# Optimization experiments

Measured on AMD Instinct MI355X. Metric: run time of the kernel, lower is better.

Reference implementation:

```python
import jax, jax.numpy as jnp
import numpy as np

B, S, HID = 2, 2048, 2048
NH, NKV = 16, 4
HD = HID // NH            # 128
N_REP = NH // NKV          # 4
THETA = 10000.0
NEG = -1e9


def _rope_tables(position_ids):
    # inv_freq: [HD/2]
    inv_freq = 1.0 / (THETA ** (jnp.arange(0, HD, 2, dtype=jnp.float32) / HD))
    freqs = position_ids.astype(jnp.float32)[..., None] * inv_freq  # [B,S,HD/2]
    emb = jnp.concatenate([freqs, freqs], axis=-1)                  # [B,S,HD]
    return jnp.cos(emb), jnp.sin(emb)


def _rotate_half(x):
    return jnp.concatenate([-x[..., HD // 2:], x[..., :HD // 2]], axis=-1)


def setup_inputs() -> dict:
    key = jax.random.key(0)
    k1, k2, k3 = jax.random.split(key, 3)
    hidden_states = jax.random.normal(k1, (B, S, HID), dtype=jnp.float32)
    w_qkv = jax.random.normal(k2, (HID + 2 * NKV * HD, HID), dtype=jnp.float32) * 0.02
    w_out = jax.random.normal(k3, (HID, HID), dtype=jnp.float32) * 0.02
    causal = jnp.tril(jnp.ones((S, S), dtype=bool))
    attention_mask = jnp.where(causal, 0.0, NEG).astype(jnp.float32)
    attention_mask = jnp.broadcast_to(attention_mask[None, None], (B, 1, S, S))
    position_ids = jnp.broadcast_to(jnp.arange(S, dtype=jnp.int64), (B, S))
    return {"hidden_states": hidden_states, "w_qkv": w_qkv, "w_out": w_out,
            "attention_mask": attention_mask, "position_ids": position_ids}


def reference(hidden_states, w_qkv, w_out, attention_mask, position_ids):
    bsz, q_len, _ = hidden_states.shape
    qkv = hidden_states @ w_qkv.T                                   # [B,S,HID+2*NKV*HD]
    q, k, v = jnp.split(qkv, [HID, HID + NKV * HD], axis=-1)
    q = q.reshape(bsz, q_len, NH, HD).transpose(0, 2, 1, 3)         # [B,NH,S,HD]
    k = k.reshape(bsz, q_len, NKV, HD).transpose(0, 2, 1, 3)        # [B,NKV,S,HD]
    v = v.reshape(bsz, q_len, NKV, HD).transpose(0, 2, 1, 3)

    cos, sin = _rope_tables(position_ids)                           # [B,S,HD]
    cos, sin = cos[:, None], sin[:, None]                           # unsqueeze head dim
    q = q * cos + _rotate_half(q) * sin
    k = k * cos + _rotate_half(k) * sin

    # GQA: repeat KV heads to match query heads (repeat_kv)
    k = jnp.repeat(k, N_REP, axis=1)                                # [B,NH,S,HD]
    v = jnp.repeat(v, N_REP, axis=1)

    scale = 1.0 / jnp.sqrt(jnp.float32(HD))
    scores = jnp.einsum('bhqd,bhkd->bhqk', q, k) * scale
    scores = scores + attention_mask                                # [B,NH,S,S]
    attn = jax.nn.softmax(scores.astype(jnp.float32), axis=-1).astype(q.dtype)
    out = jnp.einsum('bhqk,bhkd->bhqd', attn, v)                    # [B,NH,S,HD]
    out = out.transpose(0, 2, 1, 3).reshape(bsz, q_len, HID)
    return out @ w_out.T
```

## Files before the change

kernel.cpp:

```cpp
#include <hip/hip_runtime.h>
#include <hip/hip_bf16.h>
#include <math.h>

#define S_LEN   2048
#define HIDDEN  2048
#define NHEADS  16
#define NKVH    4
#define HDIM    128

typedef short  short8  __attribute__((ext_vector_type(8)));
typedef float  floatx4 __attribute__((ext_vector_type(4)));
typedef __hip_bfloat16 bf16;

__device__ inline void async_copy16(const void* g, void* l) {
  __builtin_amdgcn_global_load_lds((__attribute__((address_space(1))) void*)(g),
                                   (__attribute__((address_space(3))) void*)(l),
                                   16, 0, 0);
}

__device__ inline unsigned short cvt1(float x) {
  bf16 t = __float2bfloat16(x);
  return *reinterpret_cast<unsigned short*>(&t);
}
__device__ inline float us2f(unsigned short u) {
  unsigned int v = ((unsigned int)u) << 16;
  return *reinterpret_cast<float*>(&v);
}

#define N8_H  1048576
#define N8_WQ  786432
#define N8_WO  524288
__global__ __launch_bounds__(256) void cvt_all(const float* __restrict__ h,
                                               const float* __restrict__ wq,
                                               const float* __restrict__ wo,
                                               unsigned short* __restrict__ dst) {
  const int i = blockIdx.x * 256 + threadIdx.x;
  if (i >= N8_H + N8_WQ + N8_WO) return;
  const float* src; int j;
  if (i < N8_H)              { src = h;  j = i; }
  else if (i < N8_H + N8_WQ) { src = wq; j = i - N8_H; }
  else                       { src = wo; j = i - N8_H - N8_WQ; }
  const float4 a = reinterpret_cast<const float4*>(src)[j * 2];
  const float4 b = reinterpret_cast<const float4*>(src)[j * 2 + 1];
  unsigned short o[8] = {cvt1(a.x), cvt1(a.y), cvt1(a.z), cvt1(a.w),
                         cvt1(b.x), cvt1(b.y), cvt1(b.z), cvt1(b.w)};
  *reinterpret_cast<short8*>(dst + (size_t)i * 8) = *reinterpret_cast<short8*>(o);
}

__global__ __launch_bounds__(256) void cvt_wo(const float* __restrict__ wo,
                                              unsigned short* __restrict__ dst) {
  const int i = blockIdx.x * 256 + threadIdx.x;
  if (i >= N8_WO) return;
  const float4 a = reinterpret_cast<const float4*>(wo)[i * 2];
  const float4 b = reinterpret_cast<const float4*>(wo)[i * 2 + 1];
  unsigned short o[8] = {cvt1(a.x), cvt1(a.y), cvt1(a.z), cvt1(a.w),
                         cvt1(b.x), cvt1(b.y), cvt1(b.z), cvt1(b.w)};
  *reinterpret_cast<short8*>(dst + (size_t)i * 8) = *reinterpret_cast<short8*>(o);
}

template<int MODE>
__global__ __launch_bounds__(512, 2) void gemm8(const bf16* __restrict__ A,
                                                const bf16* __restrict__ B,
                                                bf16* __restrict__ qbuf,
                                                bf16* __restrict__ kbuf,
                                                bf16* __restrict__ vtbuf,
                                                float* __restrict__ Cout)
{
  constexpr int K      = 2048;
  constexpr int BM     = (MODE == 0) ? 256 : 128;
  constexpr int BN     = 256;
  constexpr int MF     = BM / 32;
  constexpr int AI     = BM / 128;
  constexpr int ABYTES = BM * 64;
  constexpr int SLOT   = (BM + BN) * 64;
  constexpr int NSTEP  = K / 32;

  __shared__ __align__(16) unsigned short smem[SLOT * 4 / 2];
  char* smb = (char*)smem;

  const int bn = blockIdx.x, bm = blockIdx.y;
  const int t = threadIdx.x, w = t >> 6, lane = t & 63;
  const int m16 = lane & 15, quad = lane >> 4;
  const int wmr = (w >> 2) * (BM / 2);
  const int wn  = w & 3;

  int bcol[4];
#pragma unroll
  for (int ni = 0; ni < 4; ++ni)
    bcol[ni] = (MODE == 0)
             ? ((wn >> 1) * 128 + (wn & 1) * 32 + (ni & 1) * 16 + (ni >> 1) * 64)
             : (wn * 64 + ni * 16);

  int afo[MF], bfo[4];
#pragma unroll
  for (int mf = 0; mf < MF; ++mf) {
    const int r = wmr + mf * 16 + m16;
    afo[mf] = r * 64 + ((quad ^ ((r >> 1) & 3)) << 4);
  }
#pragma unroll
  for (int ni = 0; ni < 4; ++ni) {
    const int r = bcol[ni] + m16;
    bfo[ni] = ABYTES + r * 64 + ((quad ^ ((r >> 1) & 3)) << 4);
  }

  const bf16* srcA[AI]; int dstA[AI];
#pragma unroll
  for (int j = 0; j < AI; ++j) {
    const int ci  = w * AI + j;
    const int row = ci * 16 + (lane >> 2);
    const int sl  = (lane & 3) ^ ((row >> 1) & 3);
    srcA[j] = A + (size_t)(bm * BM + row) * K + sl * 8;
    dstA[j] = ci * 1024;
  }
  const bf16* srcB[2]; int dstB[2];
#pragma unroll
  for (int j = 0; j < 2; ++j) {
    const int ci  = w * 2 + j;
    const int row = ci * 16 + (lane >> 2);
    const int sl  = (lane & 3) ^ ((row >> 1) & 3);
    srcB[j] = B + (size_t)(bn * BN + row) * K + sl * 8;
    dstB[j] = ABYTES + ci * 1024;
  }

  auto stage = [&](int step, int slotbyte) {
#pragma unroll
    for (int j = 0; j < AI; ++j)
      async_copy16(srcA[j] + step * 32, smb + slotbyte + dstA[j]);
#pragma unroll
    for (int j = 0; j < 2; ++j)
      async_copy16(srcB[j] + step * 32, smb + slotbyte + dstB[j]);
  };

  const floatx4 zf = {0.f, 0.f, 0.f, 0.f};
  floatx4 acc[MF][4];
#pragma unroll
  for (int mf = 0; mf < MF; ++mf)
#pragma unroll
    for (int ni = 0; ni < 4; ++ni) acc[mf][ni] = zf;

  stage(0, 0); stage(1, SLOT); stage(2, 2 * SLOT);

#pragma unroll 4
  for (int s = 0; s < NSTEP; ++s) {
    __builtin_amdgcn_sched_barrier(0);
    if constexpr (MODE == 0) asm volatile("s_waitcnt vmcnt(8)" ::: "memory");
    else                     asm volatile("s_waitcnt vmcnt(6)" ::: "memory");
    __builtin_amdgcn_s_barrier();
    __builtin_amdgcn_sched_barrier(0);
    const int sb = (s & 3) * SLOT;
    short8 af[MF], bfr[4];
#pragma unroll
    for (int mf = 0; mf < MF; ++mf)
      af[mf] = *reinterpret_cast<const short8*>(smb + sb + afo[mf]);
#pragma unroll
    for (int ni = 0; ni < 4; ++ni)
      bfr[ni] = *reinterpret_cast<const short8*>(smb + sb + bfo[ni]);
    stage((s + 3) & (NSTEP - 1), ((s + 3) & 3) * SLOT);
    __builtin_amdgcn_s_setprio(1);
#pragma unroll
    for (int mf = 0; mf < MF; ++mf)
#pragma unroll
      for (int ni = 0; ni < 4; ++ni)
        acc[mf][ni] = __builtin_amdgcn_mfma_f32_16x16x32_bf16(af[mf], bfr[ni], acc[mf][ni], 0, 0, 0);
    __builtin_amdgcn_s_setprio(0);
  }
  __builtin_amdgcn_s_waitcnt(0);

  if constexpr (MODE == 1) {
#pragma unroll
    for (int mf = 0; mf < MF; ++mf)
#pragma unroll
      for (int ni = 0; ni < 4; ++ni) {
        const int row0 = bm * BM + wmr + mf * 16 + quad * 4;
        const int col  = bn * BN + bcol[ni] + m16;
#pragma unroll
        for (int r = 0; r < 4; ++r)
          Cout[(size_t)(row0 + r) * HIDDEN + col] = acc[mf][ni][r];
      }
  } else {
    const int colbase = bn * BN;
    if (colbase < HIDDEN + NKVH * HDIM) {
      const bool isQ = (colbase < HIDDEN);
      const float post = isQ ? 0.08838834764831845f : 1.0f;
      float invf[2];
#pragma unroll
      for (int p = 0; p < 2; ++p)
        invf[p] = exp2f((float)((wn & 1) * 32 + p * 16 + m16) * -0.2076205059f);
#pragma unroll
      for (int mf = 0; mf < MF; ++mf) {
        const int row0 = bm * BM + wmr + mf * 16 + quad * 4;
#pragma unroll
        for (int r = 0; r < 4; ++r) {
          const int m = row0 + r;
          const int b = m >> 11, s = m & 2047;
          float sn[2], cs[2];
          __sincosf((float)s * invf[0], &sn[0], &cs[0]);
          __sincosf((float)s * invf[1], &sn[1], &cs[1]);
#pragma unroll
          for (int ni = 0; ni < 4; ++ni) {
            const int p = ni & 1;
            const float v  = acc[mf][ni][r];
            const float v2 = acc[mf][ni ^ 2][r];
            const float rot = ((ni < 2) ? (v * cs[p] - v2 * sn[p])
                                        : (v * cs[p] + v2 * sn[p])) * post;
            const int col = colbase + bcol[ni] + m16;
            if (isQ) {
              const int hh = col >> 7, d = col & 127;
              qbuf[(((size_t)(b * NHEADS + hh)) * S_LEN + s) * HDIM + d] = __float2bfloat16(rot);
            } else {
              const int nn = col - HIDDEN; const int hh = nn >> 7, d = nn & 127;
              kbuf[(((size_t)(b * NKVH + hh)) * S_LEN + s) * HDIM + d] = __float2bfloat16(rot);
            }
          }
        }
      }
    } else {
#pragma unroll
      for (int mf = 0; mf < MF; ++mf)
#pragma unroll
        for (int ni = 0; ni < 4; ++ni) {
          const int col = colbase + bcol[ni] + m16;
          const int nn = col - HIDDEN - NKVH * HDIM;
          const int hh = nn >> 7, d = nn & 127;
          const int row0 = bm * BM + wmr + mf * 16 + quad * 4;
#pragma unroll
          for (int r = 0; r < 4; ++r) {
            const int m = row0 + r;
            const int b = m >> 11, s = m & 2047;
            vtbuf[(((size_t)(b * NKVH + hh)) * HDIM + d) * S_LEN + s] =
                __float2bfloat16(acc[mf][ni][r]);
          }
        }
    }
  }
}

__global__ __launch_bounds__(256) void attn_partial(const bf16* __restrict__ qbuf,
                                                    const bf16* __restrict__ kbuf,
                                                    const bf16* __restrict__ vtbuf,
                                                    unsigned short* __restrict__ pnum,
                                                    float* __restrict__ plsum,
                                                    bf16* __restrict__ abuf)
{
  __shared__ unsigned short Ks[2][4096];
  __shared__ unsigned short Vs[2][4096];
  __shared__ unsigned short Ps[4][1280];
  const int sidx = 159 - blockIdx.x;
  int i2, c, nch;
  if (sidx < 16)      { i2 = sidx;                       c = 0;           nch = 1; }
  else if (sidx < 48) { const int q = sidx - 16; i2 = 16 + (q >> 1); c = q & 1; nch = 2; }
  else if (sidx < 96) { const int q = sidx - 48; i2 = 32 + q / 3;    c = q % 3; nch = 3; }
  else                { const int q = sidx - 96; i2 = 48 + (q >> 2); c = q & 3; nch = 4; }
  const int len = i2 + 1;
  const int k0 = (c * len) / nch, k1 = ((c + 1) * len) / nch;
  const int kvh = blockIdx.y, b = blockIdx.z;
  const int t = threadIdx.x, w = t >> 6, lane = t & 63;
  const int m16 = lane & 15, quad = lane >> 4;
  const int h = kvh * 4 + w;

  const bf16* Qp = qbuf + (((size_t)(b * NHEADS + h)) * S_LEN + i2 * 32 + m16) * HDIM;
  short8 qf[2][4];
#pragma unroll
  for (int T = 0; T < 2; ++T)
#pragma unroll
    for (int cc = 0; cc < 4; ++cc)
      qf[T][cc] = *reinterpret_cast<const short8*>(Qp + (size_t)T * 16 * HDIM + cc * 32 + quad * 8);

  const bf16* Kp  = kbuf  + ((size_t)(b * NKVH + kvh)) * S_LEN * HDIM;
  const bf16* Vtp = vtbuf + ((size_t)(b * NKVH + kvh)) * HDIM * S_LEN;

  const int kk = lane >> 4, cK = lane & 15;
  const int rKa = w * 8 + kk, rKb = rKa + 4;
  const int offKa = rKa * 128 + ((cK ^ (rKa & 7)) * 8);
  const int offKb = rKb * 128 + ((cK ^ (rKb & 7)) * 8);
  const int dd = lane >> 2, cV = lane & 3;
  const int dVa = w * 32 + dd, dVb = dVa + 16;
  const int offVa = dVa * 2048 + ((cV ^ ((dVa >> 1) & 3)) * 8);
  const int offVb = dVb * 2048 + ((cV ^ ((dVb >> 1) & 3)) * 8);

  const floatx4 zf = {0.f, 0.f, 0.f, 0.f};
  floatx4 oacc[2][8];
#pragma unroll
  for (int T = 0; T < 2; ++T)
#pragma unroll
    for (int d = 0; d < 8; ++d) oacc[T][d] = zf;
  floatx4 lacc[2] = {zf, zf};
  unsigned short ones_s[8] = {0x3F80,0x3F80,0x3F80,0x3F80,0x3F80,0x3F80,0x3F80,0x3F80};
  const short8 ones = *reinterpret_cast<short8*>(ones_s);

  unsigned short* Pw = &Ps[w][0];

  {
    const int ks = k0 * 32;
    async_copy16(Kp + (size_t)ks * 128 + offKa, &Ks[0][w * 1024]);
    async_copy16(Kp + (size_t)ks * 128 + offKb, &Ks[0][w * 1024 + 512]);
    async_copy16(Vtp + ks + offVa, &Vs[0][w * 1024]);
    async_copy16(Vtp + ks + offVb, &Vs[0][w * 1024 + 512]);
  }
  __syncthreads();

  for (int ki = k0; ki < k1; ++ki) {
    const int buf = (ki - k0) & 1;
    if (ki + 1 < k1) {
      const int ks = (ki + 1) * 32;
      async_copy16(Kp + (size_t)ks * 128 + offKa, &Ks[buf ^ 1][w * 1024]);
      async_copy16(Kp + (size_t)ks * 128 + offKb, &Ks[buf ^ 1][w * 1024 + 512]);
      async_copy16(Vtp + ks + offVa, &Vs[buf ^ 1][w * 1024]);
      async_copy16(Vtp + ks + offVb, &Vs[buf ^ 1][w * 1024 + 512]);
    }
    const int ks = ki * 32;
    floatx4 s00 = zf, s01 = zf, s10 = zf, s11 = zf;
#pragma unroll
    for (int cc = 0; cc < 4; ++cc) {
      const int sw = ((cc * 4 + quad) ^ (m16 & 7)) * 8;
      short8 kf0 = *reinterpret_cast<const short8*>(&Ks[buf][m16 * 128 + sw]);
      short8 kf1 = *reinterpret_cast<const short8*>(&Ks[buf][(16 + m16) * 128 + sw]);
      s00 = __builtin_amdgcn_mfma_f32_16x16x32_bf16(qf[0][cc], kf0, s00, 0, 0, 0);
      s01 = __builtin_amdgcn_mfma_f32_16x16x32_bf16(qf[0][cc], kf1, s01, 0, 0, 0);
      s10 = __builtin_amdgcn_mfma_f32_16x16x32_bf16(qf[1][cc], kf0, s10, 0, 0, 0);
      s11 = __builtin_amdgcn_mfma_f32_16x16x32_bf16(qf[1][cc], kf1, s11, 0, 0, 0);
    }
#pragma unroll
    for (int T = 0; T < 2; ++T) {
      const floatx4& sa = T ? s10 : s00;
      const floatx4& sb = T ? s11 : s01;
#pragma unroll
      for (int r = 0; r < 4; ++r) {
        const int row = i2 * 32 + T * 16 + quad * 4 + r;
        const float p0 = (ks + m16      > row) ? 0.f : __expf(sa[r]);
        const float p1 = (ks + 16 + m16 > row) ? 0.f : __expf(sb[r]);
        Pw[(T * 16 + quad * 4 + r) * 40 + m16]      = cvt1(p0);
        Pw[(T * 16 + quad * 4 + r) * 40 + 16 + m16] = cvt1(p1);
      }
    }
    const short8 pa0 = *reinterpret_cast<const short8*>(&Pw[m16 * 40 + quad * 8]);
    const short8 pa1 = *reinterpret_cast<const short8*>(&Pw[(16 + m16) * 40 + quad * 8]);
    lacc[0] = __builtin_amdgcn_mfma_f32_16x16x32_bf16(pa0, ones, lacc[0], 0, 0, 0);
    lacc[1] = __builtin_amdgcn_mfma_f32_16x16x32_bf16(pa1, ones, lacc[1], 0, 0, 0);
#pragma unroll
    for (int dt = 0; dt < 8; ++dt) {
      short8 vfr = *reinterpret_cast<const short8*>(
          &Vs[buf][(dt * 16 + m16) * 32 + ((quad ^ ((m16 >> 1) & 3)) * 8)]);
      oacc[0][dt] = __builtin_amdgcn_mfma_f32_16x16x32_bf16(pa0, vfr, oacc[0][dt], 0, 0, 0);
      oacc[1][dt] = __builtin_amdgcn_mfma_f32_16x16x32_bf16(pa1, vfr, oacc[1][dt], 0, 0, 0);
    }
    __syncthreads();
  }

  if (nch == 1) {
#pragma unroll
    for (int T = 0; T < 2; ++T) {
      float invl[4];
#pragma unroll
      for (int r = 0; r < 4; ++r) invl[r] = 1.0f / lacc[T][r];
      bf16* op = abuf + (((size_t)b * S_LEN + i2 * 32 + T * 16 + quad * 4) * NHEADS + h) * HDIM + m16;
#pragma unroll
      for (int dt = 0; dt < 8; ++dt)
#pragma unroll
        for (int r = 0; r < 4; ++r)
          op[(size_t)r * NHEADS * HDIM + dt * 16] = __float2bfloat16(oacc[T][dt][r] * invl[r]);
    }
  } else {
    const int base = (i2 < 32) ? (i2 - 16) * 2
                   : (i2 < 48) ? 32 + (i2 - 32) * 3
                               : 80 + (i2 - 48) * 4;
    const int slot = (b * NHEADS + h) * 144 + base + c;
    unsigned short* np = pnum + (size_t)slot * 4096;
#pragma unroll
    for (int T = 0; T < 2; ++T)
#pragma unroll
      for (int dt = 0; dt < 8; ++dt)
#pragma unroll
        for (int r = 0; r < 4; ++r)
          np[(T * 16 + quad * 4 + r) * 128 + dt * 16 + m16] = cvt1(oacc[T][dt][r]);
    if (m16 == 0) {
#pragma unroll
      for (int T = 0; T < 2; ++T)
#pragma unroll
        for (int r = 0; r < 4; ++r)
          plsum[slot * 32 + T * 16 + quad * 4 + r] = lacc[T][r];
    }
  }
}

__global__ __launch_bounds__(256) void attn_combine(const unsigned short* __restrict__ pnum,
                                                    const float* __restrict__ plsum,
                                                    bf16* __restrict__ abuf)
{
  const int i2 = 16 + blockIdx.x;
  const int h = blockIdx.y, b = blockIdx.z;
  const int nch  = (i2 >= 48) ? 4 : (i2 >= 32) ? 3 : 2;
  const int base = (i2 < 32) ? (i2 - 16) * 2
                 : (i2 < 48) ? 32 + (i2 - 32) * 3
                             : 80 + (i2 - 48) * 4;
  const int hb = (b * NHEADS + h) * 144 + base;
  const int t = threadIdx.x, row16 = t >> 4, c0 = (t & 15) * 8;
#pragma unroll
  for (int T = 0; T < 2; ++T) {
    const int lr = T * 16 + row16;
    float acc[8] = {0.f,0.f,0.f,0.f,0.f,0.f,0.f,0.f};
    float lsum = 0.f;
    for (int c = 0; c < nch; ++c) {
      const unsigned short* np = pnum + (size_t)(hb + c) * 4096 + lr * 128 + c0;
      const short8 v = *reinterpret_cast<const short8*>(np);
#pragma unroll
      for (int j = 0; j < 8; ++j) acc[j] += us2f(((unsigned short*)&v)[j]);
      lsum += plsum[(hb + c) * 32 + lr];
    }
    const float invl = 1.0f / lsum;
    unsigned short o[8];
#pragma unroll
    for (int j = 0; j < 8; ++j) o[j] = cvt1(acc[j] * invl);
    *reinterpret_cast<short8*>(abuf + (((size_t)b * S_LEN + i2 * 32 + lr) * NHEADS + h) * HDIM + c0)
        = *reinterpret_cast<short8*>(o);
  }
}

extern "C" void kernel_launch(void* const* d_in, const int* in_sizes, int n_in,
                              void* d_out, int out_size, void* d_ws, size_t ws_size,
                              hipStream_t stream) {
  const float* hidden_f = (const float*)d_in[0];
  const float* wqkv_f   = (const float*)d_in[1];
  const float* wout_f   = (const float*)d_in[2];
  float* out = (float*)d_out;

  char* ws = (char*)d_ws;
  bf16* hbf    = (bf16*)(ws);
  bf16* wqkvbf = (bf16*)(ws + 16777216);
  bf16* woutbf = (bf16*)(ws + 29360128);
  bf16* qbuf   = (bf16*)(ws + 37748736);
  bf16* kbuf   = (bf16*)(ws + 54525952);
  bf16* vtbuf  = (bf16*)(ws + 58720256);
  bf16* abuf   = (bf16*)(ws + 62914560);
  unsigned short* pnum = (unsigned short*)(ws);
  float* plsum = (float*)(ws + 79691776);

  cvt_all<<<9216, 256, 0, stream>>>(hidden_f, wqkv_f, wout_f, (unsigned short*)ws);

  gemm8<0><<<dim3(12, 16), 512, 0, stream>>>(hbf, wqkvbf, 4096 ? qbuf : qbuf, kbuf, vtbuf, nullptr);
  attn_partial<<<dim3(160, 4, 2), 256, 0, stream>>>(qbuf, kbuf, vtbuf, pnum, plsum, abuf);
  attn_combine<<<dim3(48, 16, 2), 256, 0, stream>>>(pnum, plsum, abuf);
  cvt_wo<<<2048, 256, 0, stream>>>(wout_f, (unsigned short*)(ws + 29360128));
  gemm8<1><<<dim3(8, 32), 512, 0, stream>>>(abuf, woutbf, nullptr, nullptr, nullptr, out);
}
```

Baseline: 308.5 us.

## Widen attention blocks to 64 query rows with 8 waves sharing K/V tiles

The attention partial kernel now processes 64 query rows per block using 512 threads (8 waves: 4 heads × 2 row halves), so each K/V tile loaded into LDS serves twice as many query rows. The work split, partial-sum slot layout and combine kernel are remapped to the new 64-row granularity. This halves K/V global traffic per query row but also halves the block count, which may reduce occupancy and load balance on a large GPU.

```diff
diff --git a/kernel.cpp b/kernel.cpp
--- a/kernel.cpp
+++ b/kernel.cpp
@@ -235,7 +235,7 @@
   }
 }
 
-__global__ __launch_bounds__(256) void attn_partial(const bf16* __restrict__ qbuf,
+__global__ __launch_bounds__(512) void attn_partial(const bf16* __restrict__ qbuf,
                                                     const bf16* __restrict__ kbuf,
                                                     const bf16* __restrict__ vtbuf,
                                                     unsigned short* __restrict__ pnum,
@@ -244,21 +244,23 @@
 {
   __shared__ unsigned short Ks[2][4096];
   __shared__ unsigned short Vs[2][4096];
-  __shared__ unsigned short Ps[4][1280];
-  const int sidx = 159 - blockIdx.x;
-  int i2, c, nch;
-  if (sidx < 16)      { i2 = sidx;                       c = 0;           nch = 1; }
-  else if (sidx < 48) { const int q = sidx - 16; i2 = 16 + (q >> 1); c = q & 1; nch = 2; }
-  else if (sidx < 96) { const int q = sidx - 48; i2 = 32 + q / 3;    c = q % 3; nch = 3; }
-  else                { const int q = sidx - 96; i2 = 48 + (q >> 2); c = q & 3; nch = 4; }
-  const int len = i2 + 1;
+  __shared__ unsigned short Ps[8][1280];
+  const int sidx = 79 - blockIdx.x;
+  int i4, c, nch;
+  if (sidx < 8)       { i4 = sidx;                    c = 0;         nch = 1; }
+  else if (sidx < 24) { const int q = sidx - 8;  i4 = 8  + (q >> 1); c = q & 1; nch = 2; }
+  else if (sidx < 48) { const int q = sidx - 24; i4 = 16 + q / 3;    c = q % 3; nch = 3; }
+  else                { const int q = sidx - 48; i4 = 24 + (q >> 2); c = q & 3; nch = 4; }
+  const int len = 2 * (i4 + 1);
   const int k0 = (c * len) / nch, k1 = ((c + 1) * len) / nch;
   const int kvh = blockIdx.y, b = blockIdx.z;
   const int t = threadIdx.x, w = t >> 6, lane = t & 63;
   const int m16 = lane & 15, quad = lane >> 4;
-  const int h = kvh * 4 + w;
-
-  const bf16* Qp = qbuf + (((size_t)(b * NHEADS + h)) * S_LEN + i2 * 32 + m16) * HDIM;
+  const int half = w >> 2;
+  const int h = kvh * 4 + (w & 3);
+  const int qrow0 = i4 * 64 + half * 32;
+
+  const bf16* Qp = qbuf + (((size_t)(b * NHEADS + h)) * S_LEN + qrow0 + m16) * HDIM;
   short8 qf[2][4];
 #pragma unroll
   for (int T = 0; T < 2; ++T)
@@ -269,14 +271,12 @@
   const bf16* Kp  = kbuf  + ((size_t)(b * NKVH + kvh)) * S_LEN * HDIM;
   const bf16* Vtp = vtbuf + ((size_t)(b * NKVH + kvh)) * HDIM * S_LEN;
 
-  const int kk = lane >> 4, cK = lane & 15;
-  const int rKa = w * 8 + kk, rKb = rKa + 4;
-  const int offKa = rKa * 128 + ((cK ^ (rKa & 7)) * 8);
-  const int offKb = rKb * 128 + ((cK ^ (rKb & 7)) * 8);
-  const int dd = lane >> 2, cV = lane & 3;
-  const int dVa = w * 32 + dd, dVb = dVa + 16;
-  const int offVa = dVa * 2048 + ((cV ^ ((dVa >> 1) & 3)) * 8);
-  const int offVb = dVb * 2048 + ((cV ^ ((dVb >> 1) & 3)) * 8);
+  const int rK = w * 4 + (lane >> 4);
+  const int cK = lane & 15;
+  const int offK = rK * 128 + ((cK ^ (rK & 7)) * 8);
+  const int dV = w * 16 + (lane >> 2);
+  const int cV = lane & 3;
+  const int offV = dV * 2048 + ((cV ^ ((dV >> 1) & 3)) * 8);
 
   const floatx4 zf = {0.f, 0.f, 0.f, 0.f};
   floatx4 oacc[2][8];
@@ -292,10 +292,8 @@
 
   {
     const int ks = k0 * 32;
-    async_copy16(Kp + (size_t)ks * 128 + offKa, &Ks[0][w * 1024]);
-    async_copy16(Kp + (size_t)ks * 128 + offKb, &Ks[0][w * 1024 + 512]);
-    async_copy16(Vtp + ks + offVa, &Vs[0][w * 1024]);
-    async_copy16(Vtp + ks + offVb, &Vs[0][w * 1024 + 512]);
+    async_copy16(Kp + (size_t)ks * 128 + offK, &Ks[0][w * 512]);
+    async_copy16(Vtp + ks + offV, &Vs[0][w * 512]);
   }
   __syncthreads();
 
@@ -303,10 +301,8 @@
     const int buf = (ki - k0) & 1;
     if (ki + 1 < k1) {
       const int ks = (ki + 1) * 32;
-      async_copy16(Kp + (size_t)ks * 128 + offKa, &Ks[buf ^ 1][w * 1024]);
-      async_copy16(Kp + (size_t)ks * 128 + offKb, &Ks[buf ^ 1][w * 1024 + 512]);
-      async_copy16(Vtp + ks + offVa, &Vs[buf ^ 1][w * 1024]);
-      async_copy16(Vtp + ks + offVb, &Vs[buf ^ 1][w * 1024 + 512]);
+      async_copy16(Kp + (size_t)ks * 128 + offK, &Ks[buf ^ 1][w * 512]);
+      async_copy16(Vtp + ks + offV, &Vs[buf ^ 1][w * 512]);
     }
     const int ks = ki * 32;
     floatx4 s00 = zf, s01 = zf, s10 = zf, s11 = zf;
@@ -326,7 +322,7 @@
       const floatx4& sb = T ? s11 : s01;
 #pragma unroll
       for (int r = 0; r < 4; ++r) {
-        const int row = i2 * 32 + T * 16 + quad * 4 + r;
+        const int row = qrow0 + T * 16 + quad * 4 + r;
         const float p0 = (ks + m16      > row) ? 0.f : __expf(sa[r]);
         const float p1 = (ks + 16 + m16 > row) ? 0.f : __expf(sb[r]);
         Pw[(T * 16 + quad * 4 + r) * 40 + m16]      = cvt1(p0);
@@ -353,7 +349,7 @@
       float invl[4];
 #pragma unroll
       for (int r = 0; r < 4; ++r) invl[r] = 1.0f / lacc[T][r];
-      bf16* op = abuf + (((size_t)b * S_LEN + i2 * 32 + T * 16 + quad * 4) * NHEADS + h) * HDIM + m16;
+      bf16* op = abuf + (((size_t)b * S_LEN + qrow0 + T * 16 + quad * 4) * NHEADS + h) * HDIM + m16;
 #pragma unroll
       for (int dt = 0; dt < 8; ++dt)
 #pragma unroll
@@ -361,24 +357,24 @@
           op[(size_t)r * NHEADS * HDIM + dt * 16] = __float2bfloat16(oacc[T][dt][r] * invl[r]);
     }
   } else {
-    const int base = (i2 < 32) ? (i2 - 16) * 2
-                   : (i2 < 48) ? 32 + (i2 - 32) * 3
-                               : 80 + (i2 - 48) * 4;
-    const int slot = (b * NHEADS + h) * 144 + base + c;
-    unsigned short* np = pnum + (size_t)slot * 4096;
+    const int base = (i4 < 16) ? (i4 - 8) * 2
+                   : (i4 < 24) ? 16 + (i4 - 16) * 3
+                               : 40 + (i4 - 24) * 4;
+    const int slot = (b * NHEADS + h) * 72 + base + c;
+    unsigned short* np = pnum + (size_t)slot * 8192;
 #pragma unroll
     for (int T = 0; T < 2; ++T)
 #pragma unroll
       for (int dt = 0; dt < 8; ++dt)
 #pragma unroll
         for (int r = 0; r < 4; ++r)
-          np[(T * 16 + quad * 4 + r) * 128 + dt * 16 + m16] = cvt1(oacc[T][dt][r]);
+          np[(half * 32 + T * 16 + quad * 4 + r) * 128 + dt * 16 + m16] = cvt1(oacc[T][dt][r]);
     if (m16 == 0) {
 #pragma unroll
       for (int T = 0; T < 2; ++T)
 #pragma unroll
         for (int r = 0; r < 4; ++r)
-          plsum[slot * 32 + T * 16 + quad * 4 + r] = lacc[T][r];
+          plsum[(size_t)slot * 64 + half * 32 + T * 16 + quad * 4 + r] = lacc[T][r];
     }
   }
 }
@@ -387,31 +383,31 @@
                                                     const float* __restrict__ plsum,
                                                     bf16* __restrict__ abuf)
 {
-  const int i2 = 16 + blockIdx.x;
+  const int i4 = 8 + blockIdx.x;
   const int h = blockIdx.y, b = blockIdx.z;
-  const int nch  = (i2 >= 48) ? 4 : (i2 >= 32) ? 3 : 2;
-  const int base = (i2 < 32) ? (i2 - 16) * 2
-                 : (i2 < 48) ? 32 + (i2 - 32) * 3
-                             : 80 + (i2 - 48) * 4;
-  const int hb = (b * NHEADS + h) * 144 + base;
+  const int nch  = (i4 < 16) ? 2 : (i4 < 24) ? 3 : 4;
+  const int base = (i4 < 16) ? (i4 - 8) * 2
+                 : (i4 < 24) ? 16 + (i4 - 16) * 3
+                             : 40 + (i4 - 24) * 4;
+  const int hb = (b * NHEADS + h) * 72 + base;
   const int t = threadIdx.x, row16 = t >> 4, c0 = (t & 15) * 8;
 #pragma unroll
-  for (int T = 0; T < 2; ++T) {
+  for (int T = 0; T < 4; ++T) {
     const int lr = T * 16 + row16;
     float acc[8] = {0.f,0.f,0.f,0.f,0.f,0.f,0.f,0.f};
     float lsum = 0.f;
     for (int c = 0; c < nch; ++c) {
-      const unsigned short* np = pnum + (size_t)(hb + c) * 4096 + lr * 128 + c0;
+      const unsigned short* np = pnum + (size_t)(hb + c) * 8192 + lr * 128 + c0;
       const short8 v = *reinterpret_cast<const short8*>(np);
 #pragma unroll
       for (int j = 0; j < 8; ++j) acc[j] += us2f(((unsigned short*)&v)[j]);
-      lsum += plsum[(hb + c) * 32 + lr];
+      lsum += plsum[(size_t)(hb + c) * 64 + lr];
     }
     const float invl = 1.0f / lsum;
     unsigned short o[8];
 #pragma unroll
     for (int j = 0; j < 8; ++j) o[j] = cvt1(acc[j] * invl);
-    *reinterpret_cast<short8*>(abuf + (((size_t)b * S_LEN + i2 * 32 + lr) * NHEADS + h) * HDIM + c0)
+    *reinterpret_cast<short8*>(abuf + (((size_t)b * S_LEN + i4 * 64 + lr) * NHEADS + h) * HDIM + c0)
         = *reinterpret_cast<short8*>(o);
   }
 }
@@ -437,9 +433,9 @@
 
   cvt_all<<<9216, 256, 0, stream>>>(hidden_f, wqkv_f, wout_f, (unsigned short*)ws);
 
-  gemm8<0><<<dim3(12, 16), 512, 0, stream>>>(hbf, wqkvbf, 4096 ? qbuf : qbuf, kbuf, vtbuf, nullptr);
-  attn_partial<<<dim3(160, 4, 2), 256, 0, stream>>>(qbuf, kbuf, vtbuf, pnum, plsum, abuf);
-  attn_combine<<<dim3(48, 16, 2), 256, 0, stream>>>(pnum, plsum, abuf);
+  gemm8<0><<<dim3(12, 16), 512, 0, stream>>>(hbf, wqkvbf, qbuf, kbuf, vtbuf, nullptr);
+  attn_partial<<<dim3(80, 4, 2), 512, 0, stream>>>(qbuf, kbuf, vtbuf, pnum, plsum, abuf);
+  attn_combine<<<dim3(24, 16, 2), 256, 0, stream>>>(pnum, plsum, abuf);
   cvt_wo<<<2048, 256, 0, stream>>>(wout_f, (unsigned short*)(ws + 29360128));
   gemm8<1><<<dim3(8, 32), 512, 0, stream>>>(abuf, woutbf, nullptr, nullptr, nullptr, out);
 }
```

Result: slower. 319.4 us (+3.5%).
